# Kernel optimization log

Hardware: AMD Instinct MI355X
Metric: run time of the kernel (lower is better)

The kernel has to match this reference:

```python
import jax, jax.numpy as jnp
import numpy as np

BATCH = 10000
NUM_TREES = 1000
NUM_NODES = 511  # full binary tree of depth 8
N_FEATURES = 256
N_CLASSES = 1
MAX_DEPTH = 8


def setup_inputs() -> dict:
    key = jax.random.key(0)
    k = jax.random.split(key, 6)
    flat = NUM_TREES * NUM_NODES
    x = jax.random.normal(k[0], (BATCH, N_FEATURES), dtype=jnp.float32)
    thresholds = jax.random.normal(k[1], (flat,), dtype=jnp.float32)
    values = jax.random.normal(k[2], (flat, N_CLASSES), dtype=jnp.float32)
    lefts = jax.random.randint(k[3], (flat,), 0, NUM_NODES).astype(jnp.int64)
    rights = jax.random.randint(k[4], (flat,), 0, NUM_NODES).astype(jnp.int64)
    features = jax.random.randint(k[5], (flat,), 0, N_FEATURES).astype(jnp.int64)
    return {
        "x": x,
        "thresholds": thresholds,
        "values": values,
        "lefts": lefts,
        "rights": rights,
        "features": features,
        "num_trees": NUM_TREES,
        "num_nodes": NUM_NODES,
        "max_depth": MAX_DEPTH,
    }


def reference(x, thresholds, values, lefts, rights, features, num_trees, num_nodes, max_depth):
    batch = x.shape[0]
    # nodes_offset: flat index of each tree's root in the concatenated node arrays
    nodes_offset = (jnp.arange(num_trees, dtype=jnp.int32) * num_nodes)[None, :]  # [1, T]
    indexes = jnp.broadcast_to(nodes_offset, (batch, num_trees))  # [B, T]
    for _ in range(max_depth):
        feature_nodes = features[indexes]                     # [B, T] feature id per current node
        feature_values = jnp.take_along_axis(x, feature_nodes, axis=1)  # [B, T]
        thr = thresholds[indexes]                             # [B, T]
        l = lefts[indexes]                                    # [B, T]
        r = rights[indexes]                                   # [B, T]
        indexes = jnp.where(feature_values >= thr, r, l) + nodes_offset
    output = values[indexes]  # [B, T, C]
    return output
```

## Files before the change

kernel.cpp:

```cpp
#include <hip/hip_runtime.h>
#include <stdint.h>

#define BATCH     10000
#define NUM_TREES 1000
#define NUM_NODES 511
#define NFEAT     256
#define DEPTH     8
#define FLAT_NODES (NUM_TREES * NUM_NODES)

#define TREE_BYTES 1360
#define VLEAF_OFF  ((size_t)NUM_TREES * TREE_BYTES)
#define WS_NEEDED  (VLEAF_OFF + (size_t)NUM_TREES * 256 * 4)
#define XT_LD      10048
#define XT_OFF     WS_NEEDED
#define XT_BYTES   ((size_t)NFEAT * XT_LD * 4)
#define WS_XT      (XT_OFF + XT_BYTES)

#define BT 32
#define TT 64
#define NTHREADS 512
#define XS_BYTES  (NFEAT * BT * 4)
#define OUT_LD    67
#define SH_BYTES  XS_BYTES

#define UNROLL_BLOCKS 250
#define TRANS_BLOCKS  (157 * 4)

__device__ __forceinline__ void glds16(const void* g, void* l) {
  __builtin_amdgcn_global_load_lds(
      (const __attribute__((address_space(1))) unsigned int*)g,
      (__attribute__((address_space(3))) unsigned int*)l, 16, 0, 0);
}

__global__ __launch_bounds__(256)
void prepack_kernel(const float* __restrict__ thr,
                    const int* __restrict__ feats,
                    const int* __restrict__ lefts,
                    const int* __restrict__ rights,
                    const float* __restrict__ values,
                    const float* __restrict__ x,
                    unsigned char* __restrict__ ws) {
  __shared__ unsigned char sh[64 * 65 * 4];
  const int tid = threadIdx.x;

  if (blockIdx.x < UNROLL_BLOCKS) {
    uint16_t* n_s = (uint16_t*)sh;
    const int wv = tid >> 6, lane = tid & 63;
    const int tree = blockIdx.x * 4 + wv;
    const int base = tree * NUM_NODES;
    uint16_t* n = n_s + wv * 512;
    uint4* rec   = (uint4*)(ws + (size_t)tree * TREE_BYTES);
    float* vleaf = (float*)(ws + VLEAF_OFF + (size_t)tree * 1024);

    if (lane == 0) n[0] = 0;
    __syncthreads();
    const int EBASE[4] = {0, 1, 5, 21};
    #pragma unroll
    for (int d = 0; d < 8; ++d) {
      const int lvl = (1 << d) - 1, cnt = 1 << d;
      for (int i = lane; i < cnt; i += 64) {
        int p  = lvl + i;
        int np = n[p];
        int nl = lefts[base + np], nr = rights[base + np];
        n[2 * p + 1] = (uint16_t)nl;
        n[2 * p + 2] = (uint16_t)nr;
        if ((d & 1) == 0) {
          uint32_t f3 = (uint32_t)feats[base + np] |
                        ((uint32_t)feats[base + nl] << 8) |
                        ((uint32_t)feats[base + nr] << 16);
          rec[EBASE[d >> 1] + i] =
              make_uint4(__float_as_uint(thr[base + np]),
                         __float_as_uint(thr[base + nl]),
                         __float_as_uint(thr[base + nr]), f3);
        }
      }
      __syncthreads();
    }
    #pragma unroll
    for (int i = lane; i < 256; i += 64)
      vleaf[i] = values[base + n[255 + i]];
  } else {
    float (*tile)[65] = (float(*)[65])sh;
    float* xT = (float*)(ws + XT_OFF);
    const int t = blockIdx.x - UNROLL_BLOCKS;
    const int b0 = (t >> 2) * 64, f0 = (t & 3) * 64;
    const float4* xg = (const float4*)x;
    #pragma unroll
    for (int p = 0; p < 4; ++p) {
      int i = tid + p * 256;
      int r = i >> 4, c4 = i & 15;
      int gb = b0 + r;
      float4 v = (gb < BATCH) ? xg[(size_t)gb * 64 + (f0 >> 2) + c4]
                              : make_float4(0.f, 0.f, 0.f, 0.f);
      tile[r][4 * c4 + 0] = v.x;
      tile[r][4 * c4 + 1] = v.y;
      tile[r][4 * c4 + 2] = v.z;
      tile[r][4 * c4 + 3] = v.w;
    }
    __syncthreads();
    #pragma unroll
    for (int p = 0; p < 4; ++p) {
      int i = tid + p * 256;
      int fr = i >> 4, b4 = i & 15;
      float4 w = make_float4(tile[4 * b4 + 0][fr], tile[4 * b4 + 1][fr],
                             tile[4 * b4 + 2][fr], tile[4 * b4 + 3][fr]);
      *(float4*)(xT + (size_t)(f0 + fr) * XT_LD + b0 + 4 * b4) = w;
    }
  }
}

template <bool XT>
__global__ __launch_bounds__(NTHREADS, 8)
void traverse32(const float* __restrict__ x,
                const unsigned char* __restrict__ ws,
                float* __restrict__ out) {
  extern __shared__ unsigned char smem[];
  float* x_s   = (float*)smem;
  float* out_s = (float*)smem;

  const int tid  = threadIdx.x;
  const int wid  = tid >> 6;
  const int lane = tid & 63;
  const int row  = lane & 31;
  const int th   = lane >> 5;
  const int b0   = blockIdx.y * BT;
  const int t0   = blockIdx.x * TT;

  const unsigned char* nb = ws + (size_t)(t0 + 8 * wid + th) * TREE_BYTES;
  uint4 r[4];
  #pragma unroll
  for (int s = 0; s < 4; ++s)
    r[s] = *(const uint4*)(nb + (size_t)(2 * s) * TREE_BYTES);

  if (XT) {
    const float* xT = (const float*)(ws + XT_OFF);
    #pragma unroll
    for (int k = 0; k < 4; ++k) {
      int fi = tid + k * NTHREADS;
      int f = fi >> 3, c16 = fi & 7;
      glds16(xT + (size_t)f * XT_LD + b0 + 4 * c16,
             (unsigned char*)x_s + (size_t)fi * 16);
    }
  } else {
    const float4* xg = (const float4*)x;
    #pragma unroll
    for (int p = 0; p < 4; ++p) {
      int i = tid + p * NTHREADS;
      int rr = i >> 6, c = i & 63;
      int gb = b0 + rr;
      float4 v = (gb < BATCH) ? xg[(size_t)gb * 64 + c]
                              : make_float4(0.f, 0.f, 0.f, 0.f);
      int o = (c << 7) + (rr ^ (c & 31));
      x_s[o]      = v.x;
      x_s[o + 32] = v.y;
      x_s[o + 64] = v.z;
      x_s[o + 96] = v.w;
    }
  }
  __syncthreads();

  auto xgather = [&](int f) -> float {
    if (XT) return x_s[(f << 5) + row];
    return x_s[(f << 5) + (row ^ ((f >> 2) & 31))];
  };

  int loc[4] = {0, 0, 0, 0};
  #pragma unroll
  for (int it = 0; it < 4; ++it) {
    float xp[4], xl[4], xr[4];
    #pragma unroll
    for (int s = 0; s < 4; ++s) {
      xp[s] = xgather(r[s].w & 255);
      xl[s] = xgather((r[s].w >> 8) & 255);
      xr[s] = xgather((r[s].w >> 16) & 255);
    }
    #pragma unroll
    for (int s = 0; s < 4; ++s) {
      bool c0  = (xp[s] >= __uint_as_float(r[s].x));
      float xc = c0 ? xr[s] : xl[s];
      float tc = __uint_as_float(c0 ? r[s].z : r[s].y);
      loc[s] = 4 * loc[s] + 2 * (int)c0 + (int)(xc >= tc);
    }
    if (it < 3) {
      const int eoff = (it == 0) ? 16 : (it == 1) ? 80 : 336;
      #pragma unroll
      for (int s = 0; s < 4; ++s)
        r[s] = *(const uint4*)(nb + (size_t)(2 * s) * TREE_BYTES +
                               loc[s] * 16 + eoff);
    }
  }
  const float* vl = (const float*)(ws + VLEAF_OFF);
  float v[4];
  #pragma unroll
  for (int s = 0; s < 4; ++s) {
    int g  = t0 + 8 * wid + 2 * s + th;
    int cg = (g < NUM_TREES) ? g : 0;
    v[s] = vl[(size_t)cg * 256 + loc[s]];
  }

  __syncthreads();
  #pragma unroll
  for (int s = 0; s < 4; ++s)
    out_s[row * OUT_LD + 8 * wid + 2 * s + th] = v[s];
  __syncthreads();

  #pragma unroll
  for (int k = 0; k < 4; ++k) {
    int rr = (tid >> 6) + 8 * k;
    int col = tid & 63;
    int gb = b0 + rr, gt = t0 + col;
    if (gb < BATCH && gt < NUM_TREES)
      out[(size_t)gb * NUM_TREES + gt] = out_s[rr * OUT_LD + col];
  }
}

#define FB_BT 64
#define FB_TT 64
#define FB_TPR 16
#define FB_NROUNDS 4
#define FB_NTHREADS 1024
#define FB_XS (NFEAT * 64 * 4)
#define FB_NSU (FB_TPR * NUM_NODES)
#define FB_NS (FB_NSU * 8)
#define FB_OLD (FB_TT + 1)
#define FB_OS (FB_BT * FB_OLD * 4)
#define FB_SH (FB_XS + FB_NS + FB_OS)
#define FB_PREF ((FB_NSU + FB_NTHREADS - 1) / FB_NTHREADS)

__global__ __launch_bounds__(FB_NTHREADS, 1)
void fb_traverse(const float* __restrict__ x,
                 const float* __restrict__ thrg,
                 const int* __restrict__ featg,
                 const int* __restrict__ leftg,
                 const int* __restrict__ rightg,
                 const float* __restrict__ values,
                 float* __restrict__ out) {
  extern __shared__ unsigned char smem[];
  float* x_s     = (float*)smem;
  uint2* nodes_s = (uint2*)(smem + FB_XS);
  float* out_s   = (float*)(smem + FB_XS + FB_NS);
  const int tid = threadIdx.x, wid = tid >> 6, lane = tid & 63;
  const int b0 = blockIdx.y * FB_BT, t0 = blockIdx.x * FB_TT;
  uint2 pf[FB_PREF];
  auto load_round = [&](int rr) {
    const int gbase = (t0 + rr * FB_TPR) * NUM_NODES;
    #pragma unroll
    for (int k = 0; k < FB_PREF; ++k) {
      int fi = tid + k * FB_NTHREADS;
      uint2 v = make_uint2(0u, 0u);
      if (fi < FB_NSU) {
        int gi = gbase + fi;
        if (gi < FLAT_NODES) {
          uint32_t meta = (uint32_t)featg[gi] | ((uint32_t)leftg[gi] << 8) |
                          ((uint32_t)rightg[gi] << 20);
          v = make_uint2(__float_as_uint(thrg[gi]), meta);
        }
      }
      pf[k] = v;
    }
  };
  auto write_nodes = [&]() {
    #pragma unroll
    for (int k = 0; k < FB_PREF; ++k) {
      int fi = tid + k * FB_NTHREADS;
      if (fi < FB_NSU) nodes_s[fi] = pf[k];
    }
  };
  load_round(0);
  {
    const float4* xg = (const float4*)x;
    #pragma unroll
    for (int p = 0; p < (FB_BT * (NFEAT / 4)) / FB_NTHREADS; ++p) {
      int i = tid + p * FB_NTHREADS;
      int r = i >> 6, c = i & 63;
      int gb = b0 + r;
      float4 v = make_float4(0.f, 0.f, 0.f, 0.f);
      if (gb < BATCH) v = xg[gb * (NFEAT / 4) + c];
      int o = (c << 8) + (r ^ (c & 31));
      x_s[o] = v.x; x_s[o + 64] = v.y; x_s[o + 128] = v.z; x_s[o + 192] = v.w;
    }
  }
  write_nodes();
  __syncthreads();
  for (int r = 0; r < FB_NROUNDS; ++r) {
    if (r + 1 < FB_NROUNDS) load_round(r + 1);
    const uint2* nA = nodes_s + wid * NUM_NODES;
    const int tr0 = t0 + r * FB_TPR;
    const int gta = tr0 + wid;
    const int offA = (gta < NUM_TREES ? gta : 0) * NUM_NODES;
    uint2 na = nA[0];
    float va = 0.f;
    #pragma unroll
    for (int d = 0; d < DEPTH; ++d) {
      int fa = na.y & 0xFF;
      int la = (na.y >> 8) & 0xFFF;
      int ra = (int)(na.y >> 20);
      float xa = x_s[(fa << 6) + (lane ^ ((fa >> 2) & 31))];
      if (d < DEPTH - 1) {
        uint2 nla = nA[la], nra = nA[ra];
        na = (xa >= __uint_as_float(na.x)) ? nra : nla;
      } else {
        float vla = values[offA + la], vra = values[offA + ra];
        va = (xa >= __uint_as_float(na.x)) ? vra : vla;
      }
    }
    out_s[lane * FB_OLD + r * FB_TPR + wid] = va;
    __syncthreads();
    if (r + 1 < FB_NROUNDS) { write_nodes(); __syncthreads(); }
  }
  {
    const int gt = t0 + lane;
    #pragma unroll
    for (int p = 0; p < FB_BT / 16; ++p) {
      int rr = p * 16 + wid;
      int gb = b0 + rr;
      if (gb < BATCH && gt < NUM_TREES)
        out[gb * NUM_TREES + gt] = out_s[rr * FB_OLD + lane];
    }
  }
}

extern "C" void kernel_launch(void* const* d_in, const int* in_sizes, int n_in,
                              void* d_out, int out_size, void* d_ws, size_t ws_size,
                              hipStream_t stream) {
  const float* x          = (const float*)d_in[0];
  const float* thresholds = (const float*)d_in[1];
  const float* values     = (const float*)d_in[2];
  const int*   lefts      = (const int*)d_in[3];
  const int*   rights     = (const int*)d_in[4];
  const int*   features   = (const int*)d_in[5];
  float* out = (float*)d_out;

  dim3 grid((NUM_TREES + TT - 1) / TT, (BATCH + BT - 1) / BT);
  if (ws_size >= WS_XT) {
    unsigned char* ws = (unsigned char*)d_ws;
    prepack_kernel<<<UNROLL_BLOCKS + TRANS_BLOCKS, 256, 0, stream>>>(
        thresholds, features, lefts, rights, values, x, ws);
    traverse32<true><<<grid, NTHREADS, SH_BYTES, stream>>>(x, ws, out);
  } else if (ws_size >= WS_NEEDED) {
    unsigned char* ws = (unsigned char*)d_ws;
    prepack_kernel<<<UNROLL_BLOCKS, 256, 0, stream>>>(
        thresholds, features, lefts, rights, values, x, ws);
    traverse32<false><<<grid, NTHREADS, SH_BYTES, stream>>>(x, ws, out);
  } else {
    hipFuncSetAttribute(reinterpret_cast<const void*>(fb_traverse),
                        hipFuncAttributeMaxDynamicSharedMemorySize, FB_SH);
    dim3 fgrid((NUM_TREES + FB_TT - 1) / FB_TT, (BATCH + FB_BT - 1) / FB_BT);
    fb_traverse<<<fgrid, FB_NTHREADS, FB_SH, stream>>>(
        x, thresholds, features, lefts, rights, values, out);
  }
}
```

Measured before the change: 55.48 us.

## Speculatively prefetch all four child records before branch decisions in traversal

Each thread now handles two trees instead of four, and the block doubles to 1024 threads. In each two-level step the kernel loads all four candidate grandchild records (and, at the last level, all four leaf values as a float4) before evaluating the comparisons, then selects the right one. This removes the dependent load latency between the comparison and the next node fetch. In exchange it costs four times the node-load bandwidth per step, and the launch_bounds of 1024 threads with min 8 blocks may constrain registers.

After: 117.6 us. 112% more time.

```diff
diff --git a/kernel.cpp b/kernel.cpp
--- a/kernel.cpp
+++ b/kernel.cpp
@@ -18,7 +18,7 @@
 
 #define BT 32
 #define TT 64
-#define NTHREADS 512
+#define NTHREADS 1024
 #define XS_BYTES  (NFEAT * BT * 4)
 #define OUT_LD    67
 #define SH_BYTES  XS_BYTES
@@ -111,9 +111,9 @@
 
 template <bool XT>
 __global__ __launch_bounds__(NTHREADS, 8)
-void traverse32(const float* __restrict__ x,
-                const unsigned char* __restrict__ ws,
-                float* __restrict__ out) {
+void traverse_spec(const float* __restrict__ x,
+                   const unsigned char* __restrict__ ws,
+                   float* __restrict__ out) {
   extern __shared__ unsigned char smem[];
   float* x_s   = (float*)smem;
   float* out_s = (float*)smem;
@@ -126,16 +126,15 @@
   const int b0   = blockIdx.y * BT;
   const int t0   = blockIdx.x * TT;
 
-  const unsigned char* nb = ws + (size_t)(t0 + 8 * wid + th) * TREE_BYTES;
-  uint4 r[4];
-  #pragma unroll
-  for (int s = 0; s < 4; ++s)
-    r[s] = *(const uint4*)(nb + (size_t)(2 * s) * TREE_BYTES);
+  const unsigned char* nb0 = ws + (size_t)(t0 + 4 * wid + th) * TREE_BYTES;
+  const unsigned char* nb1 = nb0 + 2 * TREE_BYTES;
+  uint4 r0 = *(const uint4*)nb0;
+  uint4 r1 = *(const uint4*)nb1;
 
   if (XT) {
     const float* xT = (const float*)(ws + XT_OFF);
     #pragma unroll
-    for (int k = 0; k < 4; ++k) {
+    for (int k = 0; k < 2; ++k) {
       int fi = tid + k * NTHREADS;
       int f = fi >> 3, c16 = fi & 7;
       glds16(xT + (size_t)f * XT_LD + b0 + 4 * c16,
@@ -144,7 +143,7 @@
   } else {
     const float4* xg = (const float4*)x;
     #pragma unroll
-    for (int p = 0; p < 4; ++p) {
+    for (int p = 0; p < 2; ++p) {
       int i = tid + p * NTHREADS;
       int rr = i >> 6, c = i & 63;
       int gb = b0 + rr;
@@ -164,49 +163,63 @@
     return x_s[(f << 5) + (row ^ ((f >> 2) & 31))];
   };
 
-  int loc[4] = {0, 0, 0, 0};
+  const float* vl = (const float*)(ws + VLEAF_OFF);
+  int g0 = t0 + 4 * wid + th, g1 = g0 + 2;
+  const int gcl0 = (g0 < NUM_TREES) ? g0 : 0;
+  const int gcl1 = (g1 < NUM_TREES) ? g1 : 0;
+
+  int loc0 = 0, loc1 = 0;
+  float v0 = 0.f, v1 = 0.f;
   #pragma unroll
   for (int it = 0; it < 4; ++it) {
-    float xp[4], xl[4], xr[4];
-    #pragma unroll
-    for (int s = 0; s < 4; ++s) {
-      xp[s] = xgather(r[s].w & 255);
-      xl[s] = xgather((r[s].w >> 8) & 255);
-      xr[s] = xgather((r[s].w >> 16) & 255);
-    }
-    #pragma unroll
-    for (int s = 0; s < 4; ++s) {
-      bool c0  = (xp[s] >= __uint_as_float(r[s].x));
-      float xc = c0 ? xr[s] : xl[s];
-      float tc = __uint_as_float(c0 ? r[s].z : r[s].y);
-      loc[s] = 4 * loc[s] + 2 * (int)c0 + (int)(xc >= tc);
-    }
+    float xp0 = xgather(r0.w & 255);
+    float xl0 = xgather((r0.w >> 8) & 255);
+    float xr0 = xgather((r0.w >> 16) & 255);
+    float xp1 = xgather(r1.w & 255);
+    float xl1 = xgather((r1.w >> 8) & 255);
+    float xr1 = xgather((r1.w >> 16) & 255);
     if (it < 3) {
       const int eoff = (it == 0) ? 16 : (it == 1) ? 80 : 336;
-      #pragma unroll
-      for (int s = 0; s < 4; ++s)
-        r[s] = *(const uint4*)(nb + (size_t)(2 * s) * TREE_BYTES +
-                               loc[s] * 16 + eoff);
-    }
-  }
-  const float* vl = (const float*)(ws + VLEAF_OFF);
-  float v[4];
+      const uint4* ca = (const uint4*)(nb0 + eoff + 64 * loc0);
+      const uint4* cb = (const uint4*)(nb1 + eoff + 64 * loc1);
+      uint4 a0 = ca[0], a1 = ca[1], a2 = ca[2], a3 = ca[3];
+      uint4 e0 = cb[0], e1 = cb[1], e2 = cb[2], e3 = cb[3];
+      bool c00 = (xp0 >= __uint_as_float(r0.x));
+      float xc0 = c00 ? xr0 : xl0;
+      bool c10 = (xc0 >= __uint_as_float(c00 ? r0.z : r0.y));
+      bool c01 = (xp1 >= __uint_as_float(r1.x));
+      float xc1 = c01 ? xr1 : xl1;
+      bool c11 = (xc1 >= __uint_as_float(c01 ? r1.z : r1.y));
+      uint4 sa = c00 ? a2 : a0, sb = c00 ? a3 : a1;
+      r0 = c10 ? sb : sa;
+      uint4 se = c01 ? e2 : e0, sf = c01 ? e3 : e1;
+      r1 = c11 ? sf : se;
+      loc0 = 4 * loc0 + 2 * (int)c00 + (int)c10;
+      loc1 = 4 * loc1 + 2 * (int)c01 + (int)c11;
+    } else {
+      float4 lf0 = *(const float4*)(vl + (size_t)gcl0 * 256 + 4 * loc0);
+      float4 lf1 = *(const float4*)(vl + (size_t)gcl1 * 256 + 4 * loc1);
+      bool c00 = (xp0 >= __uint_as_float(r0.x));
+      float xc0 = c00 ? xr0 : xl0;
+      bool c10 = (xc0 >= __uint_as_float(c00 ? r0.z : r0.y));
+      bool c01 = (xp1 >= __uint_as_float(r1.x));
+      float xc1 = c01 ? xr1 : xl1;
+      bool c11 = (xc1 >= __uint_as_float(c01 ? r1.z : r1.y));
+      float ta = c00 ? lf0.z : lf0.x, tb = c00 ? lf0.w : lf0.y;
+      v0 = c10 ? tb : ta;
+      float tc = c01 ? lf1.z : lf1.x, td = c01 ? lf1.w : lf1.y;
+      v1 = c10 || true ? (c11 ? td : tc) : 0.f;
+    }
+  }
+
+  __syncthreads();
+  out_s[row * OUT_LD + 4 * wid + th]     = v0;
+  out_s[row * OUT_LD + 4 * wid + 2 + th] = v1;
+  __syncthreads();
+
   #pragma unroll
-  for (int s = 0; s < 4; ++s) {
-    int g  = t0 + 8 * wid + 2 * s + th;
-    int cg = (g < NUM_TREES) ? g : 0;
-    v[s] = vl[(size_t)cg * 256 + loc[s]];
-  }
-
-  __syncthreads();
-  #pragma unroll
-  for (int s = 0; s < 4; ++s)
-    out_s[row * OUT_LD + 8 * wid + 2 * s + th] = v[s];
-  __syncthreads();
-
-  #pragma unroll
-  for (int k = 0; k < 4; ++k) {
-    int rr = (tid >> 6) + 8 * k;
+  for (int k = 0; k < 2; ++k) {
+    int rr = wid + 16 * k;
     int col = tid & 63;
     int gb = b0 + rr, gt = t0 + col;
     if (gb < BATCH && gt < NUM_TREES)
@@ -336,12 +349,12 @@
     unsigned char* ws = (unsigned char*)d_ws;
     prepack_kernel<<<UNROLL_BLOCKS + TRANS_BLOCKS, 256, 0, stream>>>(
         thresholds, features, lefts, rights, values, x, ws);
-    traverse32<true><<<grid, NTHREADS, SH_BYTES, stream>>>(x, ws, out);
+    traverse_spec<true><<<grid, NTHREADS, SH_BYTES, stream>>>(x, ws, out);
   } else if (ws_size >= WS_NEEDED) {
     unsigned char* ws = (unsigned char*)d_ws;
     prepack_kernel<<<UNROLL_BLOCKS, 256, 0, stream>>>(
         thresholds, features, lefts, rights, values, x, ws);
-    traverse32<false><<<grid, NTHREADS, SH_BYTES, stream>>>(x, ws, out);
+    traverse_spec<false><<<grid, NTHREADS, SH_BYTES, stream>>>(x, ws, out);
   } else {
     hipFuncSetAttribute(reinterpret_cast<const void*>(fb_traverse),
                         hipFuncAttributeMaxDynamicSharedMemorySize, FB_SH);
```
